# Performance work log

Hardware: AMD Instinct MI355X
Metric: run time of the kernel (lower is better)

Reference implementation:

```python
import jax, jax.numpy as jnp
import numpy as np


def setup_inputs() -> dict:
    key = jax.random.key(0)
    B, I, H = 8192, 1024, 1024
    C = I + H
    ks = jax.random.split(key, 7)
    # Xavier-uniform bound for Linear(C, H)
    bound = float(np.sqrt(6.0 / (C + H)))
    def xavier(k):
        return jax.random.uniform(k, (H, C), jnp.float32, -bound, bound)
    return {
        "x": jax.random.normal(ks[0], (B, I), jnp.float32),
        "h": jax.random.normal(ks[1], (B, H), jnp.float32),
        "c": jax.random.normal(ks[2], (B, H), jnp.float32),
        "W_i": xavier(ks[3]),
        "W_f": xavier(ks[4]),
        "W_o": xavier(ks[5]),
        "W_g": xavier(ks[6]),
        "b_i": jnp.zeros((H,), jnp.float32),
        "b_f": jnp.zeros((H,), jnp.float32),
        "b_o": jnp.zeros((H,), jnp.float32),
        "b_g": jnp.zeros((H,), jnp.float32),
    }


def reference(x, h, c, W_i, W_f, W_o, W_g, b_i, b_f, b_o, b_g):
    # combined: [B, input+hidden]
    combined = jnp.concatenate([x, h], axis=1)
    # fuse 4 gate GEMMs into one: W stacked -> [4H, C]
    W = jnp.concatenate([W_i, W_f, W_o, W_g], axis=0)
    b = jnp.concatenate([b_i, b_f, b_o, b_g], axis=0)
    gates = combined @ W.T + b  # [B, 4H]
    i_pre, f_pre, o_pre, g_pre = jnp.split(gates, 4, axis=1)
    i = jax.nn.sigmoid(i_pre)
    f = jax.nn.sigmoid(f_pre)
    o = jax.nn.sigmoid(o_pre)
    g = jnp.tanh(g_pre)
    c_t = f * c + i * g
    h_t = o * jnp.tanh(c_t)
    return (h_t, c_t)
```

## Files before the change

### kernel.cpp

```cpp
#include <hip/hip_runtime.h>
#include <hip/hip_bf16.h>
#include <stdint.h>


typedef __bf16 bf16x8 __attribute__((ext_vector_type(8)));
typedef __bf16 bf16x4 __attribute__((ext_vector_type(4)));
typedef float f32x4 __attribute__((ext_vector_type(4)));

#define B_DIM 8192
#define H_DIM 1024
#define C_DIM 2048
#define BM 128
#define BNC 32
#define BK 64
#define K_ITERS (C_DIM / BK)

#define XH_ELEMS (B_DIM * H_DIM)
#define W_ELEMS  (H_DIM * C_DIM)
#define CVT_TOTAL (2 * XH_ELEMS + 4 * W_ELEMS)
#define WS_NEEDED ((size_t)CVT_TOTAL * 2)

__device__ __forceinline__ void async_cp16(void* lds_dst, const void* g_src) {
    __builtin_amdgcn_global_load_lds(
        (const __attribute__((address_space(1))) void*)g_src,
        (__attribute__((address_space(3))) void*)lds_dst,
        16, 0, 0);
}

__global__ __launch_bounds__(256)
void cvt_kernel(const float* __restrict__ x, const float* __restrict__ h,
                const float* __restrict__ wi, const float* __restrict__ wf,
                const float* __restrict__ wo, const float* __restrict__ wg,
                __hip_bfloat16* __restrict__ dst)
{
    const size_t t = (size_t)blockIdx.x * 256 + threadIdx.x;
    const size_t base = t * 4;
    const float* src;
    size_t off;
    if (base < (size_t)XH_ELEMS)            { src = x; off = base; }
    else if (base < (size_t)2 * XH_ELEMS)   { src = h; off = base - XH_ELEMS; }
    else {
        const size_t wb = base - (size_t)2 * XH_ELEMS;
        const int g = (int)(wb >> 21);
        off = wb & (W_ELEMS - 1);
        src = (g == 0) ? wi : (g == 1) ? wf : (g == 2) ? wo : wg;
    }
    const f32x4 v = *(const f32x4*)(src + off);
    __hip_bfloat16 tmp[4];
    tmp[0] = __float2bfloat16(v[0]);
    tmp[1] = __float2bfloat16(v[1]);
    tmp[2] = __float2bfloat16(v[2]);
    tmp[3] = __float2bfloat16(v[3]);
    *(bf16x4*)(dst + base) = *(const bf16x4*)tmp;
}

__global__ __launch_bounds__(256, 3)
void lstm_gemm_bf16(const __hip_bfloat16* __restrict__ xb,
                    const __hip_bfloat16* __restrict__ hb,
                    const __hip_bfloat16* __restrict__ Wb,
                    const float* __restrict__ c,
                    const float* __restrict__ pbi, const float* __restrict__ pbf,
                    const float* __restrict__ pbo, const float* __restrict__ pbg,
                    float* __restrict__ out)
{
    __shared__ __hip_bfloat16 As[BM][BK];
    __shared__ __hip_bfloat16 Bs[BM][BK];

    const int tid  = threadIdx.x;
    const int lane = tid & 63;
    const int wave = tid >> 6;
    const int wr   = wave >> 1;
    const int wc   = wave & 1;
    const int quad = lane >> 4;
    const int l16  = lane & 15;

    const int m_base = blockIdx.y * BM;
    const int n0     = blockIdx.x * BNC;

    const __hip_bfloat16* aSrc[4][2];
    const __hip_bfloat16* bSrc[4];
    char *aDst[4], *bDst[4];
#pragma unroll
    for (int a = 0; a < 4; ++a) {
        const int li   = a * 256 + tid;
        const int row  = li >> 3;
        const int sch  = ((li & 7) ^ (row & 7)) * 8;
        aSrc[a][0] = xb + (size_t)(m_base + row) * H_DIM + sch;
        aSrc[a][1] = hb + (size_t)(m_base + row) * H_DIM + sch;
        aDst[a]    = (char*)(&As[0][0]) + (size_t)li * 16;
        const int gate = (row >> 4) & 3;
        const int grow = n0 + ((row >> 6) << 4) + (row & 15);
        bSrc[a] = Wb + (size_t)gate * W_ELEMS + (size_t)grow * C_DIM + sch;
        bDst[a] = (char*)(&Bs[0][0]) + (size_t)li * 16;
    }

    int aRow[4], bRow[4];
#pragma unroll
    for (int i = 0; i < 4; ++i) aRow[i] = wr * 64 + i * 16 + l16;
#pragma unroll
    for (int j = 0; j < 4; ++j) bRow[j] = wc * 64 + j * 16 + l16;

    f32x4 acc[4][4];
#pragma unroll
    for (int i = 0; i < 4; ++i)
#pragma unroll
        for (int j = 0; j < 4; ++j)
            acc[i][j] = (f32x4){0.f, 0.f, 0.f, 0.f};

    for (int kt = 0; kt < K_ITERS; ++kt) {
        const int hsel = (kt >= (H_DIM / BK));
        const int koff = (kt & ((H_DIM / BK) - 1)) * BK;
#pragma unroll
        for (int a = 0; a < 4; ++a)
            async_cp16(aDst[a], aSrc[a][hsel] + koff);
#pragma unroll
        for (int a = 0; a < 4; ++a)
            async_cp16(bDst[a], bSrc[a] + kt * BK);
        __syncthreads();

#pragma unroll
        for (int s = 0; s < 2; ++s) {
            bf16x8 av[4], bv[4];
#pragma unroll
            for (int i = 0; i < 4; ++i) {
                const int r  = aRow[i];
                const int ch = (s * 4 + quad) ^ (r & 7);
                av[i] = *(const bf16x8*)((const char*)&As[0][0] + r * (BK * 2) + ch * 16);
            }
#pragma unroll
            for (int j = 0; j < 4; ++j) {
                const int r  = bRow[j];
                const int ch = (s * 4 + quad) ^ (r & 7);
                bv[j] = *(const bf16x8*)((const char*)&Bs[0][0] + r * (BK * 2) + ch * 16);
            }
#pragma unroll
            for (int i = 0; i < 4; ++i)
#pragma unroll
                for (int j = 0; j < 4; ++j)
                    acc[i][j] = __builtin_amdgcn_mfma_f32_16x16x32_bf16(
                        av[i], bv[j], acc[i][j], 0, 0, 0);
        }
        __syncthreads();
    }

    const int col = n0 + wc * 16 + l16;
    const float vbi = pbi[col];
    const float vbf = pbf[col];
    const float vbo = pbo[col];
    const float vbg = pbg[col];
    const size_t HB = (size_t)B_DIM * H_DIM;
#pragma unroll
    for (int i = 0; i < 4; ++i) {
        const int mb = m_base + wr * 64 + i * 16 + quad * 4;
#pragma unroll
        for (int r = 0; r < 4; ++r) {
            const size_t m = (size_t)(mb + r);
            const float ip = acc[i][0][r] + vbi;
            const float fp = acc[i][1][r] + vbf;
            const float op = acc[i][2][r] + vbo;
            const float gp = acc[i][3][r] + vbg;
            const float ig = 1.f / (1.f + __expf(-ip));
            const float fg = 1.f / (1.f + __expf(-fp));
            const float og = 1.f / (1.f + __expf(-op));
            const float eg = __expf(-2.f * fabsf(gp));
            const float gg = copysignf((1.f - eg) / (1.f + eg), gp);
            const float cin = c[m * H_DIM + col];
            const float ct = fg * cin + ig * gg;
            const float ec = __expf(-2.f * fabsf(ct));
            const float tc = copysignf((1.f - ec) / (1.f + ec), ct);
            out[m * H_DIM + col]      = og * tc;
            out[HB + m * H_DIM + col] = ct;
        }
    }
}

__global__ __launch_bounds__(256, 2)
void lstm_gemm_fused(const float* __restrict__ x, const float* __restrict__ h,
                     const float* __restrict__ Wi, const float* __restrict__ Wf,
                     const float* __restrict__ Wo, const float* __restrict__ Wg,
                     const float* __restrict__ c,
                     const float* __restrict__ pbi, const float* __restrict__ pbf,
                     const float* __restrict__ pbo, const float* __restrict__ pbg,
                     float* __restrict__ out)
{
    __shared__ __hip_bfloat16 As[BM][BK];
    __shared__ __hip_bfloat16 Bs[BM][BK];

    const int tid  = threadIdx.x;
    const int lane = tid & 63;
    const int wave = tid >> 6;
    const int wr   = wave >> 1;
    const int wc   = wave & 1;
    const int quad = lane >> 4;
    const int l16  = lane & 15;

    const int m_base = blockIdx.y * BM;
    const int n0     = blockIdx.x * BNC;

    const int srow = tid >> 1;
    const int scol = (tid & 1) * 32;
    const float* aS[2] = {
        x + (size_t)(m_base + srow) * H_DIM + scol,
        h + (size_t)(m_base + srow) * H_DIM + scol
    };
    const int gate = (srow >> 4) & 3;
    const int grow = n0 + ((srow >> 6) << 4) + (srow & 15);
    const float* Wsel = (gate == 0) ? Wi : (gate == 1) ? Wf : (gate == 2) ? Wo : Wg;
    const float* bS = Wsel + (size_t)grow * C_DIM + scol;

    int aRow[4], bRow[4];
#pragma unroll
    for (int i = 0; i < 4; ++i) aRow[i] = wr * 64 + i * 16 + l16;
#pragma unroll
    for (int j = 0; j < 4; ++j) bRow[j] = wc * 64 + j * 16 + l16;

    f32x4 acc[4][4];
#pragma unroll
    for (int i = 0; i < 4; ++i)
#pragma unroll
        for (int j = 0; j < 4; ++j)
            acc[i][j] = (f32x4){0.f, 0.f, 0.f, 0.f};

    for (int kt = 0; kt < K_ITERS; ++kt) {
        const int hsel = (kt >= (H_DIM / BK));
        const int koff = (kt & ((H_DIM / BK) - 1)) * BK;
        const float* ap = aS[hsel] + koff;
        const float* bp = bS + kt * BK;
        __hip_bfloat16 ta[32], tb[32];
#pragma unroll
        for (int q = 0; q < 8; ++q) {
            f32x4 a = *(const f32x4*)(ap + q * 4);
            f32x4 b = *(const f32x4*)(bp + q * 4);
            ta[q*4+0]=__float2bfloat16(a[0]); ta[q*4+1]=__float2bfloat16(a[1]);
            ta[q*4+2]=__float2bfloat16(a[2]); ta[q*4+3]=__float2bfloat16(a[3]);
            tb[q*4+0]=__float2bfloat16(b[0]); tb[q*4+1]=__float2bfloat16(b[1]);
            tb[q*4+2]=__float2bfloat16(b[2]); tb[q*4+3]=__float2bfloat16(b[3]);
        }
#pragma unroll
        for (int q = 0; q < 4; ++q) {
            const int ch  = (scol / 8) + q;
            const int sl  = ch ^ (srow & 7);
            *(bf16x8*)((char*)&As[0][0] + srow * (BK * 2) + sl * 16) = *(const bf16x8*)&ta[q * 8];
            *(bf16x8*)((char*)&Bs[0][0] + srow * (BK * 2) + sl * 16) = *(const bf16x8*)&tb[q * 8];
        }
        __syncthreads();

#pragma unroll
        for (int s = 0; s < 2; ++s) {
            bf16x8 av[4], bv[4];
#pragma unroll
            for (int i = 0; i < 4; ++i) {
                const int r  = aRow[i];
                const int ch = (s * 4 + quad) ^ (r & 7);
                av[i] = *(const bf16x8*)((const char*)&As[0][0] + r * (BK * 2) + ch * 16);
            }
#pragma unroll
            for (int j = 0; j < 4; ++j) {
                const int r  = bRow[j];
                const int ch = (s * 4 + quad) ^ (r & 7);
                bv[j] = *(const bf16x8*)((const char*)&Bs[0][0] + r * (BK * 2) + ch * 16);
            }
#pragma unroll
            for (int i = 0; i < 4; ++i)
#pragma unroll
                for (int j = 0; j < 4; ++j)
                    acc[i][j] = __builtin_amdgcn_mfma_f32_16x16x32_bf16(
                        av[i], bv[j], acc[i][j], 0, 0, 0);
        }
        __syncthreads();
    }

    const int col = n0 + wc * 16 + l16;
    const float vbi = pbi[col];
    const float vbf = pbf[col];
    const float vbo = pbo[col];
    const float vbg = pbg[col];
    const size_t HB = (size_t)B_DIM * H_DIM;
#pragma unroll
    for (int i = 0; i < 4; ++i) {
        const int mb = m_base + wr * 64 + i * 16 + quad * 4;
#pragma unroll
        for (int r = 0; r < 4; ++r) {
            const size_t m = (size_t)(mb + r);
            const float ip = acc[i][0][r] + vbi;
            const float fp = acc[i][1][r] + vbf;
            const float op = acc[i][2][r] + vbo;
            const float gp = acc[i][3][r] + vbg;
            const float ig = 1.f / (1.f + __expf(-ip));
            const float fg = 1.f / (1.f + __expf(-fp));
            const float og = 1.f / (1.f + __expf(-op));
            const float eg = __expf(-2.f * fabsf(gp));
            const float gg = copysignf((1.f - eg) / (1.f + eg), gp);
            const float cin = c[m * H_DIM + col];
            const float ct = fg * cin + ig * gg;
            const float ec = __expf(-2.f * fabsf(ct));
            const float tc = copysignf((1.f - ec) / (1.f + ec), ct);
            out[m * H_DIM + col]      = og * tc;
            out[HB + m * H_DIM + col] = ct;
        }
    }
}

extern "C" void kernel_launch(void* const* d_in, const int* in_sizes, int n_in,
                              void* d_out, int out_size, void* d_ws, size_t ws_size,
                              hipStream_t stream) {
    const float* x  = (const float*)d_in[0];
    const float* h  = (const float*)d_in[1];
    const float* c  = (const float*)d_in[2];
    const float* Wi = (const float*)d_in[3];
    const float* Wf = (const float*)d_in[4];
    const float* Wo = (const float*)d_in[5];
    const float* Wg = (const float*)d_in[6];
    const float* bi = (const float*)d_in[7];
    const float* bfp= (const float*)d_in[8];
    const float* bo = (const float*)d_in[9];
    const float* bg = (const float*)d_in[10];
    float* out = (float*)d_out;

    dim3 grid(H_DIM / BNC, B_DIM / BM);

    if (ws_size >= WS_NEEDED) {
        __hip_bfloat16* wsb = (__hip_bfloat16*)d_ws;
        cvt_kernel<<<CVT_TOTAL / 4 / 256, 256, 0, stream>>>(x, h, Wi, Wf, Wo, Wg, wsb);
        lstm_gemm_bf16<<<grid, dim3(256), 0, stream>>>(
            wsb, wsb + XH_ELEMS, wsb + 2 * (size_t)XH_ELEMS,
            c, bi, bfp, bo, bg, out);
    } else {
        lstm_gemm_fused<<<grid, dim3(256), 0, stream>>>(
            x, h, Wi, Wf, Wo, Wg, c, bi, bfp, bo, bg, out);
    }
}
```

Baseline: 307.9 us.

## Rewrite bf16 GEMM with 256x64 tiles, double-buffered LDS, and interleaved MFMA scheduling

```diff
diff --git a/kernel.cpp b/kernel.cpp
--- a/kernel.cpp
+++ b/kernel.cpp
@@ -10,10 +10,6 @@
 #define B_DIM 8192
 #define H_DIM 1024
 #define C_DIM 2048
-#define BM 128
-#define BNC 32
-#define BK 64
-#define K_ITERS (C_DIM / BK)
 
 #define XH_ELEMS (B_DIM * H_DIM)
 #define W_ELEMS  (H_DIM * C_DIM)
@@ -33,28 +29,32 @@
                 const float* __restrict__ wo, const float* __restrict__ wg,
                 __hip_bfloat16* __restrict__ dst)
 {
-    const size_t t = (size_t)blockIdx.x * 256 + threadIdx.x;
-    const size_t base = t * 4;
-    const float* src;
-    size_t off;
-    if (base < (size_t)XH_ELEMS)            { src = x; off = base; }
-    else if (base < (size_t)2 * XH_ELEMS)   { src = h; off = base - XH_ELEMS; }
-    else {
-        const size_t wb = base - (size_t)2 * XH_ELEMS;
-        const int g = (int)(wb >> 21);
-        off = wb & (W_ELEMS - 1);
-        src = (g == 0) ? wi : (g == 1) ? wf : (g == 2) ? wo : wg;
-    }
-    const f32x4 v = *(const f32x4*)(src + off);
-    __hip_bfloat16 tmp[4];
-    tmp[0] = __float2bfloat16(v[0]);
-    tmp[1] = __float2bfloat16(v[1]);
-    tmp[2] = __float2bfloat16(v[2]);
-    tmp[3] = __float2bfloat16(v[3]);
-    *(bf16x4*)(dst + base) = *(const bf16x4*)tmp;
+    const size_t stride = (size_t)gridDim.x * 256;
+    for (size_t t = (size_t)blockIdx.x * 256 + threadIdx.x;
+         t < (size_t)(CVT_TOTAL / 8); t += stride) {
+        const size_t base = t * 8;
+        const float* src;
+        size_t off;
+        if (base < (size_t)XH_ELEMS)            { src = x; off = base; }
+        else if (base < (size_t)2 * XH_ELEMS)   { src = h; off = base - XH_ELEMS; }
+        else {
+            const size_t wb = base - (size_t)2 * XH_ELEMS;
+            const int g = (int)(wb >> 21);
+            off = wb & (size_t)(W_ELEMS - 1);
+            src = (g == 0) ? wi : (g == 1) ? wf : (g == 2) ? wo : wg;
+        }
+        const f32x4 v0 = *(const f32x4*)(src + off);
+        const f32x4 v1 = *(const f32x4*)(src + off + 4);
+        __hip_bfloat16 tmp[8];
+        tmp[0] = __float2bfloat16(v0[0]); tmp[1] = __float2bfloat16(v0[1]);
+        tmp[2] = __float2bfloat16(v0[2]); tmp[3] = __float2bfloat16(v0[3]);
+        tmp[4] = __float2bfloat16(v1[0]); tmp[5] = __float2bfloat16(v1[1]);
+        tmp[6] = __float2bfloat16(v1[2]); tmp[7] = __float2bfloat16(v1[3]);
+        *(bf16x8*)(dst + base) = *(const bf16x8*)tmp;
+    }
 }
 
-__global__ __launch_bounds__(256, 3)
+__global__ __launch_bounds__(512, 2)
 void lstm_gemm_bf16(const __hip_bfloat16* __restrict__ xb,
                     const __hip_bfloat16* __restrict__ hb,
                     const __hip_bfloat16* __restrict__ Wb,
@@ -63,6 +63,205 @@
                     const float* __restrict__ pbo, const float* __restrict__ pbg,
                     float* __restrict__ out)
 {
+    __shared__ __hip_bfloat16 lds[2][2][256][64];
+    char* const ldsBase = (char*)&lds[0][0][0][0];
+
+    const int tid  = threadIdx.x;
+    const int lane = tid & 63;
+    const int wave = tid >> 6;
+    const int wr   = wave >> 2;
+    const int wc   = wave & 3;
+    const int quad = lane >> 4;
+    const int l16  = lane & 15;
+
+    const int bid = (int)blockIdx.x;
+    const int swz = (bid & 7) * 64 + (bid >> 3);
+    const int m_base = (swz >> 4) * 256;
+    const int n0     = (swz & 15) * 64;
+
+    uint32_t aOff[2][2], bOff[2][2];
+#pragma unroll
+    for (int a = 0; a < 2; ++a) {
+        const int li  = a * 512 + tid;
+        const int row = li >> 3;
+        const int sch = ((li & 7) ^ (row & 7)) * 8;
+#pragma unroll
+        for (int hh = 0; hh < 2; ++hh) {
+            aOff[hh][a] = (uint32_t)(m_base + hh * 128 + row) * H_DIM + (uint32_t)sch;
+            const int g   = (hh << 1) | ((row >> 4) & 1);
+            const int hco = ((row >> 5) << 4) | (row & 15);
+            bOff[hh][a] = (uint32_t)g * (uint32_t)W_ELEMS
+                        + (uint32_t)(n0 + hco) * (uint32_t)C_DIM + (uint32_t)sch;
+        }
+    }
+    const uint32_t dstT = (uint32_t)tid * 16u;
+
+#define STAGE_A(pO, hh, srcp, kel) do {                                                        \
+    async_cp16(ldsBase + (pO) + (hh) * 16384u + 0u    + dstT, (srcp) + aOff[hh][0] + (kel));   \
+    async_cp16(ldsBase + (pO) + (hh) * 16384u + 8192u + dstT, (srcp) + aOff[hh][1] + (kel));   \
+} while (0)
+#define STAGE_B(pO, hh, kel) do {                                                              \
+    async_cp16(ldsBase + (pO) + 32768u + (hh) * 16384u + 0u    + dstT, Wb + bOff[hh][0] + (kel)); \
+    async_cp16(ldsBase + (pO) + 32768u + (hh) * 16384u + 8192u + dstT, Wb + bOff[hh][1] + (kel)); \
+} while (0)
+
+    const uint32_t cb    = (uint32_t)((quad ^ (l16 & 7)) * 16);
+    const uint32_t aBase = (uint32_t)(wr * 64 + l16) * 128u + cb;
+    const uint32_t bBase = 32768u + (uint32_t)(wc * 32 + l16) * 128u + cb;
+
+#define LDA(dstv, pO, ihh, ii, ss) \
+    dstv = *(const bf16x8*)(ldsBase + (pO) + ((aBase + (ihh) * 16384u + (ii) * 2048u) ^ ((uint32_t)(ss) << 6)))
+#define LDB(dstv, pO, jj, ss) \
+    dstv = *(const bf16x8*)(ldsBase + (pO) + ((bBase + (((jj) >> 1)) * 16384u + ((jj) & 1) * 2048u) ^ ((uint32_t)(ss) << 6)))
+
+    f32x4 acc[8][4];
+#pragma unroll
+    for (int i = 0; i < 8; ++i)
+#pragma unroll
+        for (int j = 0; j < 4; ++j)
+            acc[i][j] = (f32x4){0.f, 0.f, 0.f, 0.f};
+
+    STAGE_A(0u, 0, xb, 0u);
+    STAGE_B(0u, 0, 0u);
+    STAGE_B(0u, 1, 0u);
+    STAGE_A(0u, 1, xb, 0u);
+    STAGE_A(65536u, 0, xb, 64u);
+    STAGE_B(65536u, 0, 64u);
+    STAGE_B(65536u, 1, 64u);
+    asm volatile("s_waitcnt vmcnt(6)" ::: "memory");
+    __builtin_amdgcn_s_barrier();
+
+    bf16x8 av[4][2], bv0[2][2], bv1[2][2];
+
+    for (int u = 0; u < 32; ++u) {
+        const uint32_t pO = (uint32_t)(u & 1) * 65536u;
+        const uint32_t qO = pO ^ 65536u;
+        const __hip_bfloat16* aS1 = (u + 1 < 16) ? xb : hb;
+        const uint32_t ak1 = (uint32_t)((u + 1) & 15) * 64u;
+        const __hip_bfloat16* aS2 = (u + 2 < 16) ? xb : hb;
+        const uint32_t ak2 = (uint32_t)((u + 2) & 15) * 64u;
+        const uint32_t bk2 = (uint32_t)(u + 2) * 64u;
+
+#pragma unroll
+        for (int i = 0; i < 4; ++i) { LDA(av[i][0], pO, 0, i, 0); LDA(av[i][1], pO, 0, i, 1); }
+#pragma unroll
+        for (int j = 0; j < 2; ++j) { LDB(bv0[j][0], pO, j, 0); LDB(bv0[j][1], pO, j, 1); }
+        if (u < 31) STAGE_A(qO, 1, aS1, ak1);
+        __builtin_amdgcn_s_barrier();
+        asm volatile("s_waitcnt lgkmcnt(0)" ::: "memory");
+        __builtin_amdgcn_sched_barrier(0);
+        __builtin_amdgcn_s_setprio(1);
+#pragma unroll
+        for (int i = 0; i < 4; ++i)
+#pragma unroll
+            for (int j = 0; j < 2; ++j) {
+                acc[i][j] = __builtin_amdgcn_mfma_f32_16x16x32_bf16(av[i][0], bv0[j][0], acc[i][j], 0, 0, 0);
+                acc[i][j] = __builtin_amdgcn_mfma_f32_16x16x32_bf16(av[i][1], bv0[j][1], acc[i][j], 0, 0, 0);
+            }
+        __builtin_amdgcn_s_setprio(0);
+        __builtin_amdgcn_s_barrier();
+
+#pragma unroll
+        for (int j = 0; j < 2; ++j) { LDB(bv1[j][0], pO, j + 2, 0); LDB(bv1[j][1], pO, j + 2, 1); }
+        if (u < 30) STAGE_A(pO, 0, aS2, ak2);
+        __builtin_amdgcn_s_barrier();
+        asm volatile("s_waitcnt lgkmcnt(0)" ::: "memory");
+        __builtin_amdgcn_sched_barrier(0);
+        __builtin_amdgcn_s_setprio(1);
+#pragma unroll
+        for (int i = 0; i < 4; ++i)
+#pragma unroll
+            for (int j = 0; j < 2; ++j) {
+                acc[i][j + 2] = __builtin_amdgcn_mfma_f32_16x16x32_bf16(av[i][0], bv1[j][0], acc[i][j + 2], 0, 0, 0);
+                acc[i][j + 2] = __builtin_amdgcn_mfma_f32_16x16x32_bf16(av[i][1], bv1[j][1], acc[i][j + 2], 0, 0, 0);
+            }
+        __builtin_amdgcn_s_setprio(0);
+        __builtin_amdgcn_s_barrier();
+
+#pragma unroll
+        for (int i = 0; i < 4; ++i) { LDA(av[i][0], pO, 1, i, 0); LDA(av[i][1], pO, 1, i, 1); }
+        if (u < 30) STAGE_B(pO, 0, bk2);
+        __builtin_amdgcn_s_barrier();
+        asm volatile("s_waitcnt lgkmcnt(0)" ::: "memory");
+        __builtin_amdgcn_sched_barrier(0);
+        __builtin_amdgcn_s_setprio(1);
+#pragma unroll
+        for (int i = 0; i < 4; ++i)
+#pragma unroll
+            for (int j = 0; j < 2; ++j) {
+                acc[i + 4][j] = __builtin_amdgcn_mfma_f32_16x16x32_bf16(av[i][0], bv0[j][0], acc[i + 4][j], 0, 0, 0);
+                acc[i + 4][j] = __builtin_amdgcn_mfma_f32_16x16x32_bf16(av[i][1], bv0[j][1], acc[i + 4][j], 0, 0, 0);
+            }
+        __builtin_amdgcn_s_setprio(0);
+        __builtin_amdgcn_s_barrier();
+
+        if (u < 30) STAGE_B(pO, 1, bk2);
+        __builtin_amdgcn_s_barrier();
+        __builtin_amdgcn_s_setprio(1);
+#pragma unroll
+        for (int i = 0; i < 4; ++i)
+#pragma unroll
+            for (int j = 0; j < 2; ++j) {
+                acc[i + 4][j + 2] = __builtin_amdgcn_mfma_f32_16x16x32_bf16(av[i][0], bv1[j][0], acc[i + 4][j + 2], 0, 0, 0);
+                acc[i + 4][j + 2] = __builtin_amdgcn_mfma_f32_16x16x32_bf16(av[i][1], bv1[j][1], acc[i + 4][j + 2], 0, 0, 0);
+            }
+        __builtin_amdgcn_s_setprio(0);
+        if (u < 30)       { asm volatile("s_waitcnt vmcnt(6)" ::: "memory"); }
+        else if (u == 30) { asm volatile("s_waitcnt vmcnt(0)" ::: "memory"); }
+        __builtin_amdgcn_s_barrier();
+    }
+
+#undef STAGE_A
+#undef STAGE_B
+#undef LDA
+#undef LDB
+
+    const int col = n0 + wc * 16 + l16;
+    const float vbi = pbi[col];
+    const float vbf = pbf[col];
+    const float vbo = pbo[col];
+    const float vbg = pbg[col];
+    const size_t HB = (size_t)B_DIM * H_DIM;
+#pragma unroll
+    for (int i = 0; i < 8; ++i) {
+        const int fb  = (i < 4) ? (wr * 64 + i * 16) : (128 + wr * 64 + (i - 4) * 16);
+        const int mb0 = m_base + fb + quad * 4;
+#pragma unroll
+        for (int r = 0; r < 4; ++r) {
+            const size_t m = (size_t)(mb0 + r);
+            const float ip = acc[i][0][r] + vbi;
+            const float fp = acc[i][1][r] + vbf;
+            const float op = acc[i][2][r] + vbo;
+            const float gp = acc[i][3][r] + vbg;
+            const float ig = 1.f / (1.f + __expf(-ip));
+            const float fg = 1.f / (1.f + __expf(-fp));
+            const float og = 1.f / (1.f + __expf(-op));
+            const float eg = __expf(-2.f * fabsf(gp));
+            const float gg = copysignf((1.f - eg) / (1.f + eg), gp);
+            const float cin = c[m * H_DIM + col];
+            const float ct = fg * cin + ig * gg;
+            const float ec = __expf(-2.f * fabsf(ct));
+            const float tc = copysignf((1.f - ec) / (1.f + ec), ct);
+            out[m * H_DIM + col]      = og * tc;
+            out[HB + m * H_DIM + col] = ct;
+        }
+    }
+}
+
+#define BM 128
+#define BNC 32
+#define BK 64
+#define K_ITERS (C_DIM / BK)
+
+__global__ __launch_bounds__(256, 2)
+void lstm_gemm_fused(const float* __restrict__ x, const float* __restrict__ h,
+                     const float* __restrict__ Wi, const float* __restrict__ Wf,
+                     const float* __restrict__ Wo, const float* __restrict__ Wg,
+                     const float* __restrict__ c,
+                     const float* __restrict__ pbi, const float* __restrict__ pbf,
+                     const float* __restrict__ pbo, const float* __restrict__ pbg,
+                     float* __restrict__ out)
+{
     __shared__ __hip_bfloat16 As[BM][BK];
     __shared__ __hip_bfloat16 Bs[BM][BK];
 
@@ -77,22 +276,16 @@
     const int m_base = blockIdx.y * BM;
     const int n0     = blockIdx.x * BNC;
 
-    const __hip_bfloat16* aSrc[4][2];
-    const __hip_bfloat16* bSrc[4];
-    char *aDst[4], *bDst[4];
-#pragma unroll
-    for (int a = 0; a < 4; ++a) {
-        const int li   = a * 256 + tid;
-        const int row  = li >> 3;
-        const int sch  = ((li & 7) ^ (row & 7)) * 8;
-        aSrc[a][0] = xb + (size_t)(m_base + row) * H_DIM + sch;
-        aSrc[a][1] = hb + (size_t)(m_base + row) * H_DIM + sch;
-        aDst[a]    = (char*)(&As[0][0]) + (size_t)li * 16;
-        const int gate = (row >> 4) & 3;
-        const int grow = n0 + ((row >> 6) << 4) + (row & 15);
-        bSrc[a] = Wb + (size_t)gate * W_ELEMS + (size_t)grow * C_DIM + sch;
-        bDst[a] = (char*)(&Bs[0][0]) + (size_t)li * 16;
-    }
+    const int srow = tid >> 1;
+    const int scol = (tid & 1) * 32;
+    const float* aS[2] = {
+        x + (size_t)(m_base + srow) * H_DIM + scol,
+        h + (size_t)(m_base + srow) * H_DIM + scol
+    };
+    const int gate = (srow >> 4) & 3;
+    const int grow = n0 + ((srow >> 6) << 4) + (srow & 15);
+    const float* Wsel = (gate == 0) ? Wi : (gate == 1) ? Wf : (gate == 2) ? Wo : Wg;
+    const float* bS = Wsel + (size_t)grow * C_DIM + scol;
 
     int aRow[4], bRow[4];
 #pragma unroll
@@ -110,12 +303,25 @@
     for (int kt = 0; kt < K_ITERS; ++kt) {
         const int hsel = (kt >= (H_DIM / BK));
         const int koff = (kt & ((H_DIM / BK) - 1)) * BK;
-#pragma unroll
-        for (int a = 0; a < 4; ++a)
-            async_cp16(aDst[a], aSrc[a][hsel] + koff);
-#pragma unroll
-        for (int a = 0; a < 4; ++a)
-            async_cp16(bDst[a], bSrc[a] + kt * BK);
+        const float* ap = aS[hsel] + koff;
+        const float* bp = bS + kt * BK;
+        __hip_bfloat16 ta[32], tb[32];
+#pragma unroll
+        for (int q = 0; q < 8; ++q) {
+            f32x4 a = *(const f32x4*)(ap + q * 4);
+            f32x4 b = *(const f32x4*)(bp + q * 4);
+            ta[q*4+0]=__float2bfloat16(a[0]); ta[q*4+1]=__float2bfloat16(a[1]);
+            ta[q*4+2]=__float2bfloat16(a[2]); ta[q*4+3]=__float2bfloat16(a[3]);
+            tb[q*4+0]=__float2bfloat16(b[0]); tb[q*4+1]=__float2bfloat16(b[1]);
+            tb[q*4+2]=__float2bfloat16(b[2]); tb[q*4+3]=__float2bfloat16(b[3]);
+        }
+#pragma unroll
+        for (int q = 0; q < 4; ++q) {
+            const int ch  = (scol / 8) + q;
+            const int sl  = ch ^ (srow & 7);
+            *(bf16x8*)((char*)&As[0][0] + srow * (BK * 2) + sl * 16) = *(const bf16x8*)&ta[q * 8];
+            *(bf16x8*)((char*)&Bs[0][0] + srow * (BK * 2) + sl * 16) = *(const bf16x8*)&tb[q * 8];
+        }
         __syncthreads();
 
 #pragma unroll
@@ -174,133 +380,6 @@
     }
 }
 
-__global__ __launch_bounds__(256, 2)
-void lstm_gemm_fused(const float* __restrict__ x, const float* __restrict__ h,
-                     const float* __restrict__ Wi, const float* __restrict__ Wf,
-                     const float* __restrict__ Wo, const float* __restrict__ Wg,
-                     const float* __restrict__ c,
-                     const float* __restrict__ pbi, const float* __restrict__ pbf,
-                     const float* __restrict__ pbo, const float* __restrict__ pbg,
-                     float* __restrict__ out)
-{
-    __shared__ __hip_bfloat16 As[BM][BK];
-    __shared__ __hip_bfloat16 Bs[BM][BK];
-
-    const int tid  = threadIdx.x;
-    const int lane = tid & 63;
-    const int wave = tid >> 6;
-    const int wr   = wave >> 1;
-    const int wc   = wave & 1;
-    const int quad = lane >> 4;
-    const int l16  = lane & 15;
-
-    const int m_base = blockIdx.y * BM;
-    const int n0     = blockIdx.x * BNC;
-
-    const int srow = tid >> 1;
-    const int scol = (tid & 1) * 32;
-    const float* aS[2] = {
-        x + (size_t)(m_base + srow) * H_DIM + scol,
-        h + (size_t)(m_base + srow) * H_DIM + scol
-    };
-    const int gate = (srow >> 4) & 3;
-    const int grow = n0 + ((srow >> 6) << 4) + (srow & 15);
-    const float* Wsel = (gate == 0) ? Wi : (gate == 1) ? Wf : (gate == 2) ? Wo : Wg;
-    const float* bS = Wsel + (size_t)grow * C_DIM + scol;
-
-    int aRow[4], bRow[4];
-#pragma unroll
-    for (int i = 0; i < 4; ++i) aRow[i] = wr * 64 + i * 16 + l16;
-#pragma unroll
-    for (int j = 0; j < 4; ++j) bRow[j] = wc * 64 + j * 16 + l16;
-
-    f32x4 acc[4][4];
-#pragma unroll
-    for (int i = 0; i < 4; ++i)
-#pragma unroll
-        for (int j = 0; j < 4; ++j)
-            acc[i][j] = (f32x4){0.f, 0.f, 0.f, 0.f};
-
-    for (int kt = 0; kt < K_ITERS; ++kt) {
-        const int hsel = (kt >= (H_DIM / BK));
-        const int koff = (kt & ((H_DIM / BK) - 1)) * BK;
-        const float* ap = aS[hsel] + koff;
-        const float* bp = bS + kt * BK;
-        __hip_bfloat16 ta[32], tb[32];
-#pragma unroll
-        for (int q = 0; q < 8; ++q) {
-            f32x4 a = *(const f32x4*)(ap + q * 4);
-            f32x4 b = *(const f32x4*)(bp + q * 4);
-            ta[q*4+0]=__float2bfloat16(a[0]); ta[q*4+1]=__float2bfloat16(a[1]);
-            ta[q*4+2]=__float2bfloat16(a[2]); ta[q*4+3]=__float2bfloat16(a[3]);
-            tb[q*4+0]=__float2bfloat16(b[0]); tb[q*4+1]=__float2bfloat16(b[1]);
-            tb[q*4+2]=__float2bfloat16(b[2]); tb[q*4+3]=__float2bfloat16(b[3]);
-        }
-#pragma unroll
-        for (int q = 0; q < 4; ++q) {
-            const int ch  = (scol / 8) + q;
-            const int sl  = ch ^ (srow & 7);
-            *(bf16x8*)((char*)&As[0][0] + srow * (BK * 2) + sl * 16) = *(const bf16x8*)&ta[q * 8];
-            *(bf16x8*)((char*)&Bs[0][0] + srow * (BK * 2) + sl * 16) = *(const bf16x8*)&tb[q * 8];
-        }
-        __syncthreads();
-
-#pragma unroll
-        for (int s = 0; s < 2; ++s) {
-            bf16x8 av[4], bv[4];
-#pragma unroll
-            for (int i = 0; i < 4; ++i) {
-                const int r  = aRow[i];
-                const int ch = (s * 4 + quad) ^ (r & 7);
-                av[i] = *(const bf16x8*)((const char*)&As[0][0] + r * (BK * 2) + ch * 16);
-            }
-#pragma unroll
-            for (int j = 0; j < 4; ++j) {
-                const int r  = bRow[j];
-                const int ch = (s * 4 + quad) ^ (r & 7);
-                bv[j] = *(const bf16x8*)((const char*)&Bs[0][0] + r * (BK * 2) + ch * 16);
-            }
-#pragma unroll
-            for (int i = 0; i < 4; ++i)
-#pragma unroll
-                for (int j = 0; j < 4; ++j)
-                    acc[i][j] = __builtin_amdgcn_mfma_f32_16x16x32_bf16(
-                        av[i], bv[j], acc[i][j], 0, 0, 0);
-        }
-        __syncthreads();
-    }
-
-    const int col = n0 + wc * 16 + l16;
-    const float vbi = pbi[col];
-    const float vbf = pbf[col];
-    const float vbo = pbo[col];
-    const float vbg = pbg[col];
-    const size_t HB = (size_t)B_DIM * H_DIM;
-#pragma unroll
-    for (int i = 0; i < 4; ++i) {
-        const int mb = m_base + wr * 64 + i * 16 + quad * 4;
-#pragma unroll
-        for (int r = 0; r < 4; ++r) {
-            const size_t m = (size_t)(mb + r);
-            const float ip = acc[i][0][r] + vbi;
-            const float fp = acc[i][1][r] + vbf;
-            const float op = acc[i][2][r] + vbo;
-            const float gp = acc[i][3][r] + vbg;
-            const float ig = 1.f / (1.f + __expf(-ip));
-            const float fg = 1.f / (1.f + __expf(-fp));
-            const float og = 1.f / (1.f + __expf(-op));
-            const float eg = __expf(-2.f * fabsf(gp));
-            const float gg = copysignf((1.f - eg) / (1.f + eg), gp);
-            const float cin = c[m * H_DIM + col];
-            const float ct = fg * cin + ig * gg;
-            const float ec = __expf(-2.f * fabsf(ct));
-            const float tc = copysignf((1.f - ec) / (1.f + ec), ct);
-            out[m * H_DIM + col]      = og * tc;
-            out[HB + m * H_DIM + col] = ct;
-        }
-    }
-}
-
 extern "C" void kernel_launch(void* const* d_in, const int* in_sizes, int n_in,
                               void* d_out, int out_size, void* d_ws, size_t ws_size,
                               hipStream_t stream) {
@@ -317,16 +396,14 @@
     const float* bg = (const float*)d_in[10];
     float* out = (float*)d_out;
 
-    dim3 grid(H_DIM / BNC, B_DIM / BM);
-
     if (ws_size >= WS_NEEDED) {
         __hip_bfloat16* wsb = (__hip_bfloat16*)d_ws;
-        cvt_kernel<<<CVT_TOTAL / 4 / 256, 256, 0, stream>>>(x, h, Wi, Wf, Wo, Wg, wsb);
-        lstm_gemm_bf16<<<grid, dim3(256), 0, stream>>>(
+        cvt_kernel<<<2048, 256, 0, stream>>>(x, h, Wi, Wf, Wo, Wg, wsb);
+        lstm_gemm_bf16<<<512, 512, 0, stream>>>(
             wsb, wsb + XH_ELEMS, wsb + 2 * (size_t)XH_ELEMS,
             c, bi, bfp, bo, bg, out);
     } else {
-        lstm_gemm_fused<<<grid, dim3(256), 0, stream>>>(
+        lstm_gemm_fused<<<dim3(H_DIM / BNC, B_DIM / BM), dim3(256), 0, stream>>>(
             x, h, Wi, Wf, Wo, Wg, c, bi, bfp, bo, bg, out);
     }
 }
```

Result: no change. 308.8 us (+0.3%).
